# Performance work log

Hardware: AMD Instinct MI355X
Metric: run time of the kernel (lower is better)

## Reference

```python
import jax, jax.numpy as jnp
import numpy as np

NHEADS = 16
HEAD_DIM = 128
HIDDEN = 2048
SOFTCAP = 50.0
ROPE_BASE = 10000.0
SCALE = 256.0 ** (-0.5)  # hardcoded in original, NOT head_dim**-0.5


def _rope_tables(T, D, dtype):
    inv_freq = 1.0 / (ROPE_BASE ** (jnp.arange(0, D, 2, dtype=jnp.float32) / D))
    pos = jnp.arange(T, dtype=jnp.float32)
    freqs = pos[:, None] * inv_freq[None, :]            # [T, D/2]
    emb = jnp.concatenate([freqs, freqs], axis=-1)      # [T, D]
    # broadcast shape [1, 1, T, D] for (B, H, T, D) q/k
    return jnp.cos(emb)[None, None].astype(dtype), jnp.sin(emb)[None, None].astype(dtype)


def _rotate_half(x):
    x1, x2 = x[..., : x.shape[-1] // 2], x[..., x.shape[-1] // 2:]
    return jnp.concatenate([-x2, x1], axis=-1)


def setup_inputs() -> dict:
    key = jax.random.key(0)
    ks = jax.random.split(key, 5)
    B, T = 1, 4096
    X = jax.random.normal(ks[0], (B, T, HIDDEN), dtype=jnp.float32)
    std = 0.02
    Wq = jax.random.normal(ks[1], (HIDDEN, NHEADS * HEAD_DIM), dtype=jnp.float32) * std
    Wk = jax.random.normal(ks[2], (HIDDEN, NHEADS * HEAD_DIM), dtype=jnp.float32) * std
    Wv = jax.random.normal(ks[3], (HIDDEN, NHEADS * HEAD_DIM), dtype=jnp.float32) * std
    Wo = jax.random.normal(ks[4], (NHEADS * HEAD_DIM, HIDDEN), dtype=jnp.float32) * std
    return {"X": X, "Wq": Wq, "Wk": Wk, "Wv": Wv, "Wo": Wo}


def reference(X, Wq, Wk, Wv, Wo):
    B, T, C = X.shape
    H, D = NHEADS, HEAD_DIM
    # QKV projections -> [B, H, T, D]
    q = (X @ Wq).reshape(B, T, H, D).transpose(0, 2, 1, 3)
    k = (X @ Wk).reshape(B, T, H, D).transpose(0, 2, 1, 3)
    v = (X @ Wv).reshape(B, T, H, D).transpose(0, 2, 1, 3)
    # RoPE
    cos, sin = _rope_tables(T, D, X.dtype)
    q = q * cos + _rotate_half(q) * sin
    k = k * cos + _rotate_half(k) * sin
    # attention logits with tanh softcapping
    att = jnp.einsum("bhqd,bhkd->bhqk", q, k) * SCALE
    att = jnp.tanh(att / SOFTCAP) * SOFTCAP
    causal = jnp.tril(jnp.ones((T, T), dtype=bool))[None, None]
    att = jnp.where(causal, att, -jnp.inf)
    att = jax.nn.softmax(att, axis=-1)
    # dropout is identity (train=False)
    y = jnp.einsum("bhqk,bhkd->bhqd", att, v)
    y = y.transpose(0, 2, 1, 3).reshape(B, T, H * D)
    return y @ Wo
```

## Files before the change

### kernel.cpp

```cpp
#include <hip/hip_runtime.h>
#include <stdint.h>

#define T_SEQ 4096
#define HID   2048
#define NH    16
#define HD    128

typedef __attribute__((ext_vector_type(8))) short short8;
typedef __attribute__((ext_vector_type(4))) short short4v;
typedef __attribute__((ext_vector_type(4))) float f32x4;

typedef __attribute__((address_space(1))) void as1_void;
typedef __attribute__((address_space(3))) void as3_void;

__device__ __forceinline__ unsigned short f2bf(float f){
  unsigned u = __builtin_bit_cast(unsigned, f);
  u += 0x7fffu + ((u >> 16) & 1u);
  return (unsigned short)(u >> 16);
}
__device__ __forceinline__ float bf2f(unsigned short b){
  unsigned u = ((unsigned)b) << 16;
  return __builtin_bit_cast(float, u);
}
__device__ __forceinline__ void gll16(const void* g, void* l){
  __builtin_amdgcn_global_load_lds((as1_void*)(uintptr_t)g,
                                   (as3_void*)(unsigned)(uintptr_t)l, 16, 0, 0);
}

__global__ __launch_bounds__(256) void conv_x_k(const float* __restrict__ X,
                                                unsigned short* __restrict__ O){
  int i = (blockIdx.x * 256 + threadIdx.x) * 4;
  float4 v = *(const float4*)(X + i);
  short4v o;
  o[0] = (short)f2bf(v.x); o[1] = (short)f2bf(v.y);
  o[2] = (short)f2bf(v.z); o[3] = (short)f2bf(v.w);
  *(short4v*)(O + i) = o;
}

__global__ __launch_bounds__(256) void conv_wt_k(const float* __restrict__ W0,
                                                 const float* __restrict__ W1,
                                                 const float* __restrict__ W2,
                                                 const float* __restrict__ W3,
                                                 unsigned short* __restrict__ Wt){
  const float* W = (blockIdx.z == 0) ? W0 : (blockIdx.z == 1) ? W1
                   : (blockIdx.z == 2) ? W2 : W3;
  unsigned short* out = Wt + (size_t)blockIdx.z * HID * HID;
  __shared__ float tile[32][33];
  const int x = threadIdx.x;
  const int y = threadIdx.y;
  const int k0 = blockIdx.y * 32, n0 = blockIdx.x * 32;
#pragma unroll
  for (int i = 0; i < 4; ++i){
    int r = y * 4 + i;
    tile[r][x] = W[(size_t)(k0 + r) * HID + n0 + x];
  }
  __syncthreads();
#pragma unroll
  for (int i = 0; i < 4; ++i){
    int r = y * 4 + i;
    out[(size_t)(n0 + r) * HID + k0 + x] = f2bf(tile[x][r]);
  }
}

template<int MODE, int NTOT>
__global__ __launch_bounds__(256, 3) void gemm_bt(
    const unsigned short* __restrict__ A,
    const unsigned short* __restrict__ Bt,
    unsigned short* __restrict__ Qb,
    unsigned short* __restrict__ Kb,
    unsigned short* __restrict__ Vt,
    float* __restrict__ Cf)
{
  constexpr int K = HID;
  __shared__ __align__(16) unsigned short lA[128 * 32];
  __shared__ __align__(16) unsigned short lB[128 * 32];

  const int tid  = threadIdx.x;
  const int wave = tid >> 6;
  const int lane = tid & 63;
  const int qd   = lane >> 4;
  const int mm   = lane & 15;
  const int wm   = wave >> 1;
  const int wn   = wave & 1;
  const int bm   = blockIdx.y * 128;
  const int bn   = blockIdx.x * 128;

  const unsigned short* ga[2];
  const unsigned short* gb[2];
  unsigned short* la[2];
  unsigned short* lbp[2];
#pragma unroll
  for (int i = 0; i < 2; ++i){
    int s0   = (wave * 2 + i) * 64;
    int slot = s0 + lane;
    int row  = slot >> 2;
    int kb   = (slot & 3) ^ ((row >> 1) & 3);
    ga[i]  = A  + (size_t)(bm + row) * K + kb * 8;
    gb[i]  = Bt + (size_t)(bn + row) * K + kb * 8;
    la[i]  = lA + s0 * 8;
    lbp[i] = lB + s0 * 8;
  }

  int aslot[4], bslot[4];
#pragma unroll
  for (int t = 0; t < 4; ++t){
    int ra = wm * 64 + t * 16 + mm;
    aslot[t] = ra * 4 + (qd ^ ((ra >> 1) & 3));
    int rb = wn * 64 + t * 16 + mm;
    bslot[t] = rb * 4 + (qd ^ ((rb >> 1) & 3));
  }

  const f32x4 fzero = {0.f, 0.f, 0.f, 0.f};
  f32x4 acc[4][4];
#pragma unroll
  for (int i = 0; i < 4; ++i)
#pragma unroll
    for (int j = 0; j < 4; ++j) acc[i][j] = fzero;

  for (int k0 = 0; k0 < K; k0 += 32){
    __syncthreads();
#pragma unroll
    for (int i = 0; i < 2; ++i){
      gll16(ga[i] + k0, la[i]);
      gll16(gb[i] + k0, lbp[i]);
    }
    __syncthreads();
    short8 af[4], bfv[4];
#pragma unroll
    for (int t = 0; t < 4; ++t) af[t]  = *(const short8*)(lA + aslot[t] * 8);
#pragma unroll
    for (int t = 0; t < 4; ++t) bfv[t] = *(const short8*)(lB + bslot[t] * 8);
#pragma unroll
    for (int i = 0; i < 4; ++i)
#pragma unroll
      for (int j = 0; j < 4; ++j)
        acc[i][j] = __builtin_amdgcn_mfma_f32_16x16x32_bf16(af[i], bfv[j], acc[i][j], 0, 0, 0);
  }

#pragma unroll
  for (int i = 0; i < 4; ++i){
#pragma unroll
    for (int j = 0; j < 4; ++j){
      const int col = bn + wn * 64 + j * 16 + mm;
#pragma unroll
      for (int r = 0; r < 4; ++r){
        const int row = bm + wm * 64 + i * 16 + qd * 4 + r;
        const float v = acc[i][j][r];
        if (MODE == 0){
          const int sel = col >> 11;
          const int nn  = col & 2047;
          const int h   = nn >> 7;
          const int d   = nn & 127;
          const unsigned short bv = f2bf(v);
          if (sel == 0)      Qb[((size_t)h * T_SEQ + row) * HD + d] = bv;
          else if (sel == 1) Kb[((size_t)h * T_SEQ + row) * HD + d] = bv;
          else               Vt[((size_t)(h * HD + d)) * T_SEQ + row] = bv;
        } else {
          Cf[(size_t)row * NTOT + col] = v;
        }
      }
    }
  }
}

__global__ __launch_bounds__(256) void rope_k(unsigned short* __restrict__ Qb,
                                              unsigned short* __restrict__ Kb){
  const int j = threadIdx.x & 63;
  const int t = blockIdx.x * 4 + (threadIdx.x >> 6);
  const int h = blockIdx.y;
  const float fr = (float)t * __expf(-(float)j * (9.210340371976184f / 64.f));
  const float cs = cosf(fr), sn = sinf(fr);
  const size_t base = ((size_t)h * T_SEQ + t) * HD;
  {
    float x1 = bf2f(Qb[base + j]), x2 = bf2f(Qb[base + j + 64]);
    Qb[base + j]      = f2bf(x1 * cs - x2 * sn);
    Qb[base + j + 64] = f2bf(x2 * cs + x1 * sn);
  }
  {
    float x1 = bf2f(Kb[base + j]), x2 = bf2f(Kb[base + j + 64]);
    Kb[base + j]      = f2bf(x1 * cs - x2 * sn);
    Kb[base + j + 64] = f2bf(x2 * cs + x1 * sn);
  }
}

__global__ __launch_bounds__(256, 2) void attn_k(
    const unsigned short* __restrict__ Qb,
    const unsigned short* __restrict__ Kb,
    const unsigned short* __restrict__ Vt,
    unsigned short* __restrict__ Yb)
{
  __shared__ __align__(16) unsigned char smem[73984];
  unsigned short* lKb = (unsigned short*)smem;
  unsigned short* lVb = (unsigned short*)(smem + 32768);
  unsigned short (*lP)[32][32] = (unsigned short(*)[32][32])(smem + 65536);
  float* lO = (float*)smem;
  float* lL = (float*)(smem + 65536 + 8192);

  const int tid  = threadIdx.x;
  const int w    = tid >> 6;
  const int rg   = w >> 1;
  const int kg   = w & 1;
  const int lane = tid & 63;
  const int qd   = lane >> 4;
  const int cc   = lane & 15;
  const int cx   = cc & 7;
  const int r8   = lane >> 3, c7 = lane & 7;

  const int b = blockIdx.x;
  const int h = (b & 7) + 8 * (b >> 8);
  const int pairP = (b >> 3) & 31;

  const int ce  = cc ^ qd;
  const int dlt = (ce & 4) ? -32 : 32;
  const unsigned short* gKbp = Kb + ((size_t)h * T_SEQ + w * 16 + qd) * HD + ce * 8;
  const int cV = c7 ^ r8;
  const unsigned short* gVbp = Vt + ((size_t)h * HD + w * 32 + r8) * T_SEQ + cV * 8;

  const f32x4 fzero = {0.f, 0.f, 0.f, 0.f};
  const float A0 = 0.0625f;
  const float A1 = -3.2552083e-8f;
  const float A2 = 2.0345052e-14f;

#pragma unroll 1
  for (int half = 0; half < 2; ++half){
    const int tp = half ? (63 - pairP) : pairP;
    const int qrow0 = tp * 64 + rg * 32;
    const int iters = tp + 1;

    short8 qf[2][4];
#pragma unroll
    for (int mt = 0; mt < 2; ++mt)
#pragma unroll
      for (int ks = 0; ks < 4; ++ks)
        qf[mt][ks] = *(const short8*)(Qb + ((size_t)h * T_SEQ + qrow0 + mt * 16 + cc) * HD + ks * 32 + qd * 8);

    f32x4 o[2][8];
    float lsum[2][4];
#pragma unroll
    for (int mt = 0; mt < 2; ++mt){
#pragma unroll
      for (int dn = 0; dn < 8; ++dn) o[mt][dn] = fzero;
#pragma unroll
      for (int r = 0; r < 4; ++r) lsum[mt][r] = 0.f;
    }

    {
      unsigned short* dK = lKb + w * 2048;
      unsigned short* dV = lVb + w * 2048;
#pragma unroll
      for (int i = 0; i < 4; ++i)
        gll16(gKbp + (size_t)(i * 4) * HD + ((i & 1) ? dlt : 0), dK + i * 512);
#pragma unroll
      for (int i = 0; i < 4; ++i)
        gll16(gVbp + (size_t)i * 8 * T_SEQ, dV + i * 512);
    }
    __syncthreads();

#pragma unroll 1
    for (int it = 0; it < iters; ++it){
      const int k0 = it * 64;
      if (it + 1 < iters){
        const int nb = (it + 1) & 1;
        const int kn = k0 + 64;
        unsigned short* dK = lKb + nb * 8192 + w * 2048;
        unsigned short* dV = lVb + nb * 8192 + w * 2048;
#pragma unroll
        for (int i = 0; i < 4; ++i)
          gll16(gKbp + (size_t)(kn + i * 4) * HD + ((i & 1) ? dlt : 0), dK + i * 512);
#pragma unroll
        for (int i = 0; i < 4; ++i)
          gll16(gVbp + (size_t)i * 8 * T_SEQ + kn, dV + i * 512);
      }

      const unsigned short* bK = lKb + (it & 1) * 8192;
      const unsigned short* bV = lVb + (it & 1) * 8192;

      f32x4 S[2][2];
#pragma unroll
      for (int mt = 0; mt < 2; ++mt)
#pragma unroll
        for (int nt = 0; nt < 2; ++nt) S[mt][nt] = fzero;
#pragma unroll
      for (int nt = 0; nt < 2; ++nt){
        short8 kf[4];
#pragma unroll
        for (int ks = 0; ks < 4; ++ks)
          kf[ks] = *(const short8*)(bK + ((kg * 32 + nt * 16 + cc) * 16 + ((ks * 4 + qd) ^ cx)) * 8);
#pragma unroll
        for (int mt = 0; mt < 2; ++mt)
#pragma unroll
          for (int ks = 0; ks < 4; ++ks)
            S[mt][nt] = __builtin_amdgcn_mfma_f32_16x16x32_bf16(qf[mt][ks], kf[ks], S[mt][nt], 0, 0, 0);
      }

      const bool domask = (it == iters - 1);
#pragma unroll
      for (int mt = 0; mt < 2; ++mt)
#pragma unroll
        for (int nt = 0; nt < 2; ++nt)
#pragma unroll
          for (int r = 0; r < 4; ++r){
            float s = S[mt][nt][r];
            float w2 = s * s;
            float t = fmaf(w2, A2, A1);
            t = fmaf(w2, t, A0);
            float a = s * t;
            a = fminf(fmaxf(a, -50.f), 50.f);
            float p = __expf(a);
            if (domask){
              int col = k0 + kg * 32 + nt * 16 + cc;
              int row = qrow0 + mt * 16 + qd * 4 + r;
              if (col > row) p = 0.f;
            }
            lsum[mt][r] += p;
            lP[w][mt * 16 + qd * 4 + r][nt * 16 + cc] = f2bf(p);
          }

      short8 pf[2];
#pragma unroll
      for (int mt = 0; mt < 2; ++mt)
        pf[mt] = *(const short8*)(&lP[w][mt * 16 + cc][qd * 8]);

#pragma unroll
      for (int dn = 0; dn < 8; ++dn){
        short8 vf = *(const short8*)(bV + ((dn * 16 + cc) * 8 + ((kg * 4 + qd) ^ cx)) * 8);
#pragma unroll
        for (int mt = 0; mt < 2; ++mt)
          o[mt][dn] = __builtin_amdgcn_mfma_f32_16x16x32_bf16(pf[mt], vf, o[mt][dn], 0, 0, 0);
      }
      __syncthreads();
    }

    float lred[2][4];
#pragma unroll
    for (int mt = 0; mt < 2; ++mt)
#pragma unroll
      for (int r = 0; r < 4; ++r){
        float lb = lsum[mt][r];
        lb += __shfl_xor(lb, 1);
        lb += __shfl_xor(lb, 2);
        lb += __shfl_xor(lb, 4);
        lb += __shfl_xor(lb, 8);
        lred[mt][r] = lb;
      }

    if (kg == 1){
#pragma unroll
      for (int mt = 0; mt < 2; ++mt){
#pragma unroll
        for (int dn = 0; dn < 8; ++dn)
          *(f32x4*)&lO[(dn * 16 + cc) * 68 + rg * 32 + mt * 16 + qd * 4] = o[mt][dn];
        if (cc == 0){
#pragma unroll
          for (int r = 0; r < 4; ++r)
            lL[rg * 32 + mt * 16 + qd * 4 + r] = lred[mt][r];
        }
      }
    }
    __syncthreads();
    if (kg == 0){
#pragma unroll
      for (int mt = 0; mt < 2; ++mt){
        float inv[4];
#pragma unroll
        for (int r = 0; r < 4; ++r){
          float lt = lred[mt][r] + lL[rg * 32 + mt * 16 + qd * 4 + r];
          inv[r] = __builtin_amdgcn_rcpf(lt);
        }
#pragma unroll
        for (int dn = 0; dn < 8; ++dn){
          f32x4 oo = o[mt][dn] + *(const f32x4*)&lO[(dn * 16 + cc) * 68 + rg * 32 + mt * 16 + qd * 4];
#pragma unroll
          for (int r = 0; r < 4; ++r){
            int row = qrow0 + mt * 16 + qd * 4 + r;
            Yb[(size_t)row * HID + h * HD + dn * 16 + cc] = f2bf(oo[r] * inv[r]);
          }
        }
      }
    }
    __syncthreads();
  }
}

extern "C" void kernel_launch(void* const* d_in, const int* in_sizes, int n_in,
                              void* d_out, int out_size, void* d_ws, size_t ws_size,
                              hipStream_t stream) {
  const float* X  = (const float*)d_in[0];
  const float* Wq = (const float*)d_in[1];
  const float* Wk = (const float*)d_in[2];
  const float* Wv = (const float*)d_in[3];
  const float* Wo = (const float*)d_in[4];
  float* out = (float*)d_out;

  unsigned short* ws = (unsigned short*)d_ws;
  unsigned short* Xb = ws;
  unsigned short* Wt = ws + (size_t)8  * 1024 * 1024;
  unsigned short* Qb = ws + (size_t)24 * 1024 * 1024;
  unsigned short* Kb = ws + (size_t)32 * 1024 * 1024;
  unsigned short* Vt = ws + (size_t)40 * 1024 * 1024;
  unsigned short* Yb = Xb;

  conv_x_k<<<8192, 256, 0, stream>>>(X, Xb);
  conv_wt_k<<<dim3(64, 64, 4), dim3(32, 8), 0, stream>>>(Wq, Wk, Wv, Wo, Wt);
  gemm_bt<0, 6144><<<dim3(48, 32), 256, 0, stream>>>(Xb, Wt, Qb, Kb, Vt, nullptr);
  rope_k<<<dim3(1024, NH), 256, 0, stream>>>(Qb, Kb);
  attn_k<<<dim3(512), 256, 0, stream>>>(Qb, Kb, Vt, Yb);
  gemm_bt<1, 2048><<<dim3(16, 32), 256, 0, stream>>>(Yb, Wt + (size_t)6144 * 2048,
                                                     nullptr, nullptr, nullptr, out);
}
```

Measured before the change: 473.9 us.

## Deepen GEMM K tile to 64, single-buffer attention K/V, truncate P

The projection GEMM now stages 64-wide K slices per iteration with an 8-way XOR swizzle, halving the number of barrier pairs per tile. The attention kernel drops K/V double buffering in favour of a single smaller LDS buffer loaded synchronously each iteration, which shrinks shared memory so more blocks can fit per CU but loses load/compute overlap. The probability values are truncated to bf16 rather than rounded, and the row sum accumulates the truncated value so it stays consistent with P.

```diff
diff --git a/kernel.cpp b/kernel.cpp
--- a/kernel.cpp
+++ b/kernel.cpp
@@ -72,42 +72,41 @@
     float* __restrict__ Cf)
 {
   constexpr int K = HID;
-  __shared__ __align__(16) unsigned short lA[128 * 32];
-  __shared__ __align__(16) unsigned short lB[128 * 32];
+  __shared__ __align__(16) unsigned short lA[128 * 64];
+  __shared__ __align__(16) unsigned short lB[128 * 64];
 
   const int tid  = threadIdx.x;
   const int wave = tid >> 6;
   const int lane = tid & 63;
   const int qd   = lane >> 4;
   const int mm   = lane & 15;
+  const int m7   = mm & 7;
   const int wm   = wave >> 1;
   const int wn   = wave & 1;
   const int bm   = blockIdx.y * 128;
   const int bn   = blockIdx.x * 128;
 
-  const unsigned short* ga[2];
-  const unsigned short* gb[2];
-  unsigned short* la[2];
-  unsigned short* lbp[2];
-#pragma unroll
-  for (int i = 0; i < 2; ++i){
-    int s0   = (wave * 2 + i) * 64;
+  const unsigned short* ga[4];
+  const unsigned short* gb[4];
+  unsigned short* la[4];
+  unsigned short* lbp[4];
+#pragma unroll
+  for (int i = 0; i < 4; ++i){
+    int s0   = (wave * 4 + i) * 64;
     int slot = s0 + lane;
-    int row  = slot >> 2;
-    int kb   = (slot & 3) ^ ((row >> 1) & 3);
+    int row  = slot >> 3;
+    int kb   = (slot & 7) ^ (row & 7);
     ga[i]  = A  + (size_t)(bm + row) * K + kb * 8;
     gb[i]  = Bt + (size_t)(bn + row) * K + kb * 8;
     la[i]  = lA + s0 * 8;
     lbp[i] = lB + s0 * 8;
   }
 
-  int aslot[4], bslot[4];
+  int abase[4], bbase[4];
 #pragma unroll
   for (int t = 0; t < 4; ++t){
-    int ra = wm * 64 + t * 16 + mm;
-    aslot[t] = ra * 4 + (qd ^ ((ra >> 1) & 3));
-    int rb = wn * 64 + t * 16 + mm;
-    bslot[t] = rb * 4 + (qd ^ ((rb >> 1) & 3));
+    abase[t] = (wm * 64 + t * 16 + mm) * 8;
+    bbase[t] = (wn * 64 + t * 16 + mm) * 8;
   }
 
   const f32x4 fzero = {0.f, 0.f, 0.f, 0.f};
@@ -117,24 +116,28 @@
 #pragma unroll
     for (int j = 0; j < 4; ++j) acc[i][j] = fzero;
 
-  for (int k0 = 0; k0 < K; k0 += 32){
+  for (int k0 = 0; k0 < K; k0 += 64){
     __syncthreads();
 #pragma unroll
-    for (int i = 0; i < 2; ++i){
+    for (int i = 0; i < 4; ++i){
       gll16(ga[i] + k0, la[i]);
       gll16(gb[i] + k0, lbp[i]);
     }
     __syncthreads();
-    short8 af[4], bfv[4];
-#pragma unroll
-    for (int t = 0; t < 4; ++t) af[t]  = *(const short8*)(lA + aslot[t] * 8);
-#pragma unroll
-    for (int t = 0; t < 4; ++t) bfv[t] = *(const short8*)(lB + bslot[t] * 8);
-#pragma unroll
-    for (int i = 0; i < 4; ++i)
-#pragma unroll
-      for (int j = 0; j < 4; ++j)
-        acc[i][j] = __builtin_amdgcn_mfma_f32_16x16x32_bf16(af[i], bfv[j], acc[i][j], 0, 0, 0);
+#pragma unroll
+    for (int ks = 0; ks < 2; ++ks){
+      const int co = (ks * 4 + qd) ^ m7;
+      short8 af[4], bfv[4];
+#pragma unroll
+      for (int t = 0; t < 4; ++t) af[t]  = *(const short8*)(lA + (abase[t] + co) * 8);
+#pragma unroll
+      for (int t = 0; t < 4; ++t) bfv[t] = *(const short8*)(lB + (bbase[t] + co) * 8);
+#pragma unroll
+      for (int i = 0; i < 4; ++i)
+#pragma unroll
+        for (int j = 0; j < 4; ++j)
+          acc[i][j] = __builtin_amdgcn_mfma_f32_16x16x32_bf16(af[i], bfv[j], acc[i][j], 0, 0, 0);
+    }
   }
 
 #pragma unroll
@@ -189,12 +192,12 @@
     const unsigned short* __restrict__ Vt,
     unsigned short* __restrict__ Yb)
 {
-  __shared__ __align__(16) unsigned char smem[73984];
-  unsigned short* lKb = (unsigned short*)smem;
-  unsigned short* lVb = (unsigned short*)(smem + 32768);
-  unsigned short (*lP)[32][32] = (unsigned short(*)[32][32])(smem + 65536);
+  __shared__ __align__(16) unsigned char smem[41216];
+  unsigned short* lK = (unsigned short*)smem;
+  unsigned short* lV = (unsigned short*)(smem + 16384);
+  unsigned short (*lP)[32][32] = (unsigned short(*)[32][32])(smem + 32768);
+  float* lL = (float*)(smem + 40960);
   float* lO = (float*)smem;
-  float* lL = (float*)(smem + 65536 + 8192);
 
   const int tid  = threadIdx.x;
   const int w    = tid >> 6;
@@ -244,36 +247,23 @@
       for (int r = 0; r < 4; ++r) lsum[mt][r] = 0.f;
     }
 
-    {
-      unsigned short* dK = lKb + w * 2048;
-      unsigned short* dV = lVb + w * 2048;
-#pragma unroll
-      for (int i = 0; i < 4; ++i)
-        gll16(gKbp + (size_t)(i * 4) * HD + ((i & 1) ? dlt : 0), dK + i * 512);
-#pragma unroll
-      for (int i = 0; i < 4; ++i)
-        gll16(gVbp + (size_t)i * 8 * T_SEQ, dV + i * 512);
-    }
-    __syncthreads();
-
 #pragma unroll 1
     for (int it = 0; it < iters; ++it){
       const int k0 = it * 64;
-      if (it + 1 < iters){
-        const int nb = (it + 1) & 1;
-        const int kn = k0 + 64;
-        unsigned short* dK = lKb + nb * 8192 + w * 2048;
-        unsigned short* dV = lVb + nb * 8192 + w * 2048;
+      __syncthreads();
+      {
+        const unsigned short* gK = gKbp + (size_t)k0 * HD;
+        const unsigned short* gV = gVbp + k0;
+        unsigned short* dK = lK + w * 2048;
+        unsigned short* dV = lV + w * 2048;
 #pragma unroll
         for (int i = 0; i < 4; ++i)
-          gll16(gKbp + (size_t)(kn + i * 4) * HD + ((i & 1) ? dlt : 0), dK + i * 512);
+          gll16(gK + (size_t)(i * 4) * HD + ((i & 1) ? dlt : 0), dK + i * 512);
 #pragma unroll
         for (int i = 0; i < 4; ++i)
-          gll16(gVbp + (size_t)i * 8 * T_SEQ + kn, dV + i * 512);
-      }
-
-      const unsigned short* bK = lKb + (it & 1) * 8192;
-      const unsigned short* bV = lVb + (it & 1) * 8192;
+          gll16(gV + (size_t)i * 8 * T_SEQ, dV + i * 512);
+      }
+      __syncthreads();
 
       f32x4 S[2][2];
 #pragma unroll
@@ -285,7 +275,7 @@
         short8 kf[4];
 #pragma unroll
         for (int ks = 0; ks < 4; ++ks)
-          kf[ks] = *(const short8*)(bK + ((kg * 32 + nt * 16 + cc) * 16 + ((ks * 4 + qd) ^ cx)) * 8);
+          kf[ks] = *(const short8*)(lK + ((kg * 32 + nt * 16 + cc) * 16 + ((ks * 4 + qd) ^ cx)) * 8);
 #pragma unroll
         for (int mt = 0; mt < 2; ++mt)
 #pragma unroll
@@ -312,8 +302,10 @@
               int row = qrow0 + mt * 16 + qd * 4 + r;
               if (col > row) p = 0.f;
             }
-            lsum[mt][r] += p;
-            lP[w][mt * 16 + qd * 4 + r][nt * 16 + cc] = f2bf(p);
+            unsigned u = __builtin_bit_cast(unsigned, p);
+            float pt = __builtin_bit_cast(float, u & 0xffff0000u);
+            lsum[mt][r] += pt;
+            lP[w][mt * 16 + qd * 4 + r][nt * 16 + cc] = (unsigned short)(u >> 16);
           }
 
       short8 pf[2];
@@ -323,12 +315,11 @@
 
 #pragma unroll
       for (int dn = 0; dn < 8; ++dn){
-        short8 vf = *(const short8*)(bV + ((dn * 16 + cc) * 8 + ((kg * 4 + qd) ^ cx)) * 8);
+        short8 vf = *(const short8*)(lV + ((dn * 16 + cc) * 8 + ((kg * 4 + qd) ^ cx)) * 8);
 #pragma unroll
         for (int mt = 0; mt < 2; ++mt)
           o[mt][dn] = __builtin_amdgcn_mfma_f32_16x16x32_bf16(pf[mt], vf, o[mt][dn], 0, 0, 0);
       }
-      __syncthreads();
     }
 
     float lred[2][4];
@@ -344,6 +335,7 @@
         lred[mt][r] = lb;
       }
 
+    __syncthreads();
     if (kg == 1){
 #pragma unroll
       for (int mt = 0; mt < 2; ++mt){
```

New measurement: 432.4 us. 1.1x faster.
